# Kernel tuning notes

Hardware: AMD Instinct MI355X
Metric: run time of the kernel (lower is better)

Reference implementation:

```python
import jax, jax.numpy as jnp
import numpy as np

ANG = 5
WS = 8
HEADS = 2
REF = 2  # refPos = [2, 2]
NEG_SLOPE = 0.1
EPS = 1e-5


def _rel_pos_index(ws):
    coords = np.stack(np.meshgrid(np.arange(ws), np.arange(ws), indexing='ij'))  # [2,ws,ws]
    cf = coords.reshape(2, -1)
    rel = (cf[:, :, None] - cf[:, None, :]).transpose(1, 2, 0)  # [N,N,2]
    rel[..., 0] += ws - 1
    rel[..., 1] += ws - 1
    rel[..., 0] *= 2 * ws - 1
    return jnp.asarray(rel.sum(-1))  # [N,N] int

REL_IDX = _rel_pos_index(WS)


def _ln(x, g, b):
    m = jnp.mean(x, -1, keepdims=True)
    v = jnp.var(x, -1, keepdims=True)
    return (x - m) * jax.lax.rsqrt(v + EPS) * g + b


def setup_inputs():
    key = jax.random.key(0)
    ks = jax.random.split(key, 12)
    b, an2, c, h, w = 2, 25, 32, 96, 96
    C = 2 * c
    s = 0.02
    mlp_hidden = int(C * 4.0)
    inp = {}
    inp['global_fea'] = jax.random.normal(ks[0], (b, an2, c, h, w), jnp.float32)
    inp['centra_fea'] = jax.random.normal(ks[1], (b, c, h, w), jnp.float32)
    inp['disparity'] = jax.random.uniform(ks[2], (b, 1, h, w), jnp.float32)
    inp['qkv_w'] = jax.random.normal(ks[3], (3 * C, C), jnp.float32) * s
    inp['qkv_b'] = jnp.zeros((3 * C,), jnp.float32)
    inp['proj_w'] = jax.random.normal(ks[4], (C, C), jnp.float32) * s
    inp['proj_b'] = jnp.zeros((C,), jnp.float32)
    inp['rpb_table'] = jax.random.normal(ks[5], ((2 * WS - 1) ** 2, HEADS), jnp.float32) * s
    inp['ln1_g'] = jnp.ones((C,), jnp.float32)
    inp['ln1_b'] = jnp.zeros((C,), jnp.float32)
    inp['ln2_g'] = jnp.ones((C,), jnp.float32)
    inp['ln2_b'] = jnp.zeros((C,), jnp.float32)
    inp['fc1_w'] = jax.random.normal(ks[6], (mlp_hidden, C), jnp.float32) * s
    inp['fc1_b'] = jnp.zeros((mlp_hidden,), jnp.float32)
    inp['fc2_w'] = jax.random.normal(ks[7], (C, mlp_hidden), jnp.float32) * s
    inp['fc2_b'] = jnp.zeros((C,), jnp.float32)
    inp['conv_w'] = jax.random.normal(ks[8], (c, C), jnp.float32) * s  # 1x1 conv kernel squeezed
    inp['conv_b'] = jnp.zeros((c,), jnp.float32)
    return inp


def _warp(centra_fea, disparity):
    # back-projection: bilinear warp of the central (2,2) view to all ANG*ANG views
    b, c, h, w = centra_fea.shape
    d = disparity[:, 0]  # [b,h,w]
    ys, xs = jnp.meshgrid(jnp.arange(h, dtype=jnp.float32), jnp.arange(w, dtype=jnp.float32), indexing='ij')
    offs = jnp.asarray([[u - REF, v - REF] for u in range(ANG) for v in range(ANG)], jnp.float32)  # [an2,2]
    sy = ys[None, None] + d[:, None] * offs[None, :, 0, None, None]  # [b,an2,h,w]
    sx = xs[None, None] + d[:, None] * offs[None, :, 1, None, None]
    x0f = jnp.floor(sx)
    y0f = jnp.floor(sy)
    wx = sx - x0f
    wy = sy - y0f
    x0 = jnp.clip(x0f.astype(jnp.int32), 0, w - 1)
    x1 = jnp.clip(x0 + 1, 0, w - 1)
    y0 = jnp.clip(y0f.astype(jnp.int32), 0, h - 1)
    y1 = jnp.clip(y0 + 1, 0, h - 1)
    flat = centra_fea.reshape(b, c, h * w)
    an2 = ANG * ANG

    def gather(yi, xi):
        idx = (yi * w + xi).reshape(b, 1, -1)  # [b,1,an2*h*w]
        g = jnp.take_along_axis(flat, jnp.broadcast_to(idx, (b, c, an2 * h * w)), axis=2)
        return g.reshape(b, c, an2, h, w).transpose(0, 2, 1, 3, 4)  # [b,an2,c,h,w]

    wx_ = wx[:, :, None]
    wy_ = wy[:, :, None]
    return ((1 - wy_) * (1 - wx_) * gather(y0, x0) + (1 - wy_) * wx_ * gather(y0, x1)
            + wy_ * (1 - wx_) * gather(y1, x0) + wy_ * wx_ * gather(y1, x1))


def reference(global_fea, centra_fea, disparity, qkv_w, qkv_b, proj_w, proj_b, rpb_table,
              ln1_g, ln1_b, ln2_g, ln2_b, fc1_w, fc1_b, fc2_w, fc2_b, conv_w, conv_b):
    b, an2, c, h, w = global_fea.shape
    warped = _warp(centra_fea, disparity)
    x = jnp.concatenate([global_fea, warped], axis=2)  # [b,an2,2c,h,w]
    C = 2 * c
    B = b * an2
    # 'b an2 c h w -> (b an2) (h w) c'
    x = x.reshape(B, C, h, w).transpose(0, 2, 3, 1).reshape(B, h * w, C)
    # --- Swin transformer block (shift_size=0, iteration_idx=0) ---
    shortcut = x
    xn = _ln(x, ln1_g, ln1_b).reshape(B, h, w, C)
    nh, nw = h // WS, w // WS
    xw = xn.reshape(B, nh, WS, nw, WS, C).transpose(0, 1, 3, 2, 4, 5).reshape(B * nh * nw, WS * WS, C)
    nwins, N = xw.shape[0], WS * WS
    hd = C // HEADS
    qkv = (xw @ qkv_w.T + qkv_b).reshape(nwins, N, 3, HEADS, hd).transpose(2, 0, 3, 1, 4)
    q, k, v = qkv[0], qkv[1], qkv[2]  # [nwins, heads, N, hd]
    scale = hd ** -0.5
    attn = jnp.einsum('whnd,whmd->whnm', q * scale, k)
    bias = rpb_table[REL_IDX].transpose(2, 0, 1)  # [heads,N,N]
    attn = jax.nn.softmax(attn + bias[None], axis=-1)
    out = jnp.einsum('whnm,whmd->whnd', attn, v).transpose(0, 2, 1, 3).reshape(nwins, N, C)
    out = out @ proj_w.T + proj_b
    out = out.reshape(B, nh, nw, WS, WS, C).transpose(0, 1, 3, 2, 4, 5).reshape(B, h * w, C)
    x = shortcut + out
    xm = _ln(x, ln2_g, ln2_b)
    xm = jax.nn.gelu(xm @ fc1_w.T + fc1_b, approximate=False) @ fc2_w.T + fc2_b
    x = x + xm
    # '(b an2) (h w) c -> (b an2) c h w' then 1x1 conv fuse + LeakyReLU(0.1)
    x = x.reshape(B, h, w, C)
    y = jnp.einsum('bhwc,oc->bohw', x, conv_w) + conv_b[None, :, None, None]
    y = jnp.where(y >= 0, y, NEG_SLOPE * y)
    return y.reshape(b, an2, c, h, w)
```

## Files before the change

### kernel.cpp

```cpp
#include <hip/hip_runtime.h>
#include <hip/hip_bf16.h>
#include <math.h>

#define W_    96
#define HW_   9216
#define NWIN_ 144

typedef __attribute__((ext_vector_type(4))) float          f32x4;
typedef __attribute__((ext_vector_type(8))) __bf16         bf16x8;
typedef __attribute__((ext_vector_type(8))) unsigned short u16x8;

#define MFMA(a,b,c) __builtin_amdgcn_mfma_f32_16x16x32_bf16((a),(b),(c),0,0,0)

#define WOFF_QKV  0
#define WOFF_PROJ 12288
#define WOFF_FC1  16384
#define WOFF_FC2  32768
#define WOFF_CONV 49152
#define WTOT      51200
#define POFF_QKVB  0
#define POFF_PROJB 192
#define POFF_FC1B  256
#define POFF_FC2B  512
#define POFF_CONVB 576
#define POFF_RPB   608
#define POFF_LN1G  1058
#define POFF_LN1B  1122
#define POFF_LN2G  1186
#define POFF_LN2B  1250
#define PTOT       1314

template<typename T> __device__ __forceinline__ float ldv(const T* p, long i);
template<> __device__ __forceinline__ float ldv<float>(const float* p, long i){ return p[i]; }
template<> __device__ __forceinline__ float ldv<__hip_bfloat16>(const __hip_bfloat16* p, long i){ return __bfloat162float(p[i]); }

template<typename T> __device__ __forceinline__ void stv(T* p, long i, float v);
template<> __device__ __forceinline__ void stv<float>(float* p, long i, float v){ p[i] = v; }
template<> __device__ __forceinline__ void stv<__hip_bfloat16>(__hip_bfloat16* p, long i, float v){ p[i] = __float2bfloat16(v); }

__device__ __forceinline__ bf16x8 ldbf8(const __bf16* w){
    u16x8 u = *(const u16x8*)w;
    return __builtin_bit_cast(bf16x8, u);
}

__global__ void probe_kernel(const void* ln1g, int* flag){
    if (threadIdx.x == 0){
        unsigned u = *(const unsigned*)ln1g;
        *flag = (u == 0x3F803F80u) ? 1 : 0;
    }
}

template<typename T, int WANT>
__global__ __launch_bounds__(256) void convert_params(
    const int* __restrict__ flag,
    const T* qkvw, const T* qkvb, const T* projw, const T* projb, const T* rpb,
    const T* ln1g, const T* ln1b, const T* ln2g, const T* ln2b,
    const T* fc1w, const T* fc1b, const T* fc2w, const T* fc2b,
    const T* convw, const T* convb,
    __bf16* __restrict__ wbf, float* __restrict__ pf)
{
    if (*flag != WANT) return;
    int idx = blockIdx.x*256 + threadIdx.x;
    if (idx >= WTOT + PTOT) return;
    if      (idx < 12288) wbf[WOFF_QKV  + idx]          = (__bf16)ldv(qkvw, idx);
    else if (idx < 16384) wbf[WOFF_PROJ + (idx-12288)]  = (__bf16)ldv(projw, idx-12288);
    else if (idx < 32768) wbf[WOFF_FC1  + (idx-16384)]  = (__bf16)ldv(fc1w, idx-16384);
    else if (idx < 49152) wbf[WOFF_FC2  + (idx-32768)]  = (__bf16)ldv(fc2w, idx-32768);
    else if (idx < WTOT)  wbf[WOFF_CONV + (idx-49152)]  = (__bf16)ldv(convw, idx-49152);
    else {
        int p = idx - WTOT;
        if      (p < 192)  pf[POFF_QKVB  + p]        = ldv(qkvb, p);
        else if (p < 256)  pf[POFF_PROJB + (p-192)]  = ldv(projb, p-192);
        else if (p < 512)  pf[POFF_FC1B  + (p-256)]  = ldv(fc1b, p-256);
        else if (p < 576)  pf[POFF_FC2B  + (p-512)]  = ldv(fc2b, p-512);
        else if (p < 608)  pf[POFF_CONVB + (p-576)]  = ldv(convb, p-576);
        else if (p < 1058) pf[POFF_RPB   + (p-608)]  = ldv(rpb, p-608);
        else if (p < 1122) pf[POFF_LN1G  + (p-1058)] = ldv(ln1g, p-1058);
        else if (p < 1186) pf[POFF_LN1B  + (p-1122)] = ldv(ln1b, p-1122);
        else if (p < 1250) pf[POFF_LN2G  + (p-1186)] = ldv(ln2g, p-1186);
        else               pf[POFF_LN2B  + (p-1250)] = ldv(ln2b, p-1250);
    }
}

template<typename T, int WANT>
__global__ __launch_bounds__(256) void fused_kernel(
    const int* __restrict__ flag,
    const T* __restrict__ gf, const T* __restrict__ cf, const T* __restrict__ disp,
    const __bf16* __restrict__ wbf, const float* __restrict__ pf,
    T* __restrict__ out)
{
    if (*flag != WANT) return;
    __shared__ float  xs[64*65];
    __shared__ __bf16 arena[18432];

    const int tid  = threadIdx.x;
    const int lane = tid & 63, wid = tid >> 6;
    const int g = lane >> 4, cl = lane & 15;
    const int blk  = blockIdx.x;
    const int Bidx = blk / NWIN_;
    const int wrem = blk % NWIN_;
    const int wy = wrem / 12, wx = wrem % 12;
    const int b = Bidx / 25, a = Bidx % 25;
    const int hw00 = (wy*8)*W_ + wx*8;

    __bf16* qb  = arena;
    __bf16* kb  = arena + 4608;
    __bf16* vT  = arena + 9216;
    __bf16* xnr = arena + 13824;

    float* tile  = (float*)arena;
    float* tile2 = (float*)arena + 2112;
    int*   iy0 = (int*)((char*)arena + 16896);
    int*   iy1 = iy0 + 64;
    int*   ix0 = iy1 + 64;
    int*   ix1 = ix0 + 64;
    float* fys = (float*)(ix1 + 64);
    float* fxs = fys + 64;

    if (tid < 64){
        int ty = tid >> 3, tx = tid & 7;
        int y = wy*8 + ty, x = wx*8 + tx;
        int pix = y*W_ + x;
        float d  = ldv(disp, (long)b*HW_ + pix);
        float dy = (float)(a/5 - 2), dx = (float)(a%5 - 2);
        float sy = (float)y + d*dy, sx = (float)x + d*dx;
        float y0f = floorf(sy), x0f = floorf(sx);
        fys[tid] = sy - y0f; fxs[tid] = sx - x0f;
        int y0 = min(max((int)y0f,0), W_-1);
        int x0 = min(max((int)x0f,0), W_-1);
        iy0[tid]=y0; iy1[tid]=min(y0+1,W_-1);
        ix0[tid]=x0; ix1[tid]=min(x0+1,W_-1);
    }
    {
        int p = tid & 63;
        long pixoff = hw00 + (p>>3)*W_ + (p&7);
        for (int c = tid>>6; c < 32; c += 4)
            tile[c*66 + p] = ldv(gf, (((long)b*25 + a)*32 + c)*HW_ + pixoff);
    }
    __syncthreads();

    {
        int p = tid & 63;
        float fy = fys[p], fx = fxs[p];
        float w00=(1.f-fy)*(1.f-fx), w01=(1.f-fy)*fx, w10=fy*(1.f-fx), w11=fy*fx;
        long r0 = (long)iy0[p]*W_, r1 = (long)iy1[p]*W_;
        int xa = ix0[p], xb = ix1[p];
        for (int c = tid>>6; c < 32; c += 4){
            long cb = ((long)b*32 + c)*HW_;
            float v00 = ldv(cf, cb+r0+xa), v01 = ldv(cf, cb+r0+xb);
            float v10 = ldv(cf, cb+r1+xa), v11 = ldv(cf, cb+r1+xb);
            tile2[c*66 + p] = w00*v00 + w01*v01 + w10*v10 + w11*v11;
        }
    }
    __syncthreads();

    {
        const int t = tid>>2, quad = tid&3;
        float v[16]; float sum=0.f, sq=0.f;
        #pragma unroll
        for (int j=0;j<16;++j){
            int c = quad*16+j;
            float val = (c<32) ? tile[c*66 + t] : tile2[(c-32)*66 + t];
            v[j]=val; sum+=val; sq+=val*val;
        }
        sum += __shfl_xor(sum,1); sq += __shfl_xor(sq,1);
        sum += __shfl_xor(sum,2); sq += __shfl_xor(sq,2);
        float m  = sum*(1.f/64.f);
        float rs = rsqrtf(sq*(1.f/64.f) - m*m + 1e-5f);
        #pragma unroll
        for (int j=0;j<16;++j){
            int c = quad*16+j;
            xs[t*65 + c] = v[j];
            xnr[t*72 + c] = (__bf16)((v[j]-m)*rs*pf[POFF_LN1G+c] + pf[POFF_LN1B+c]);
        }
    }
    __syncthreads();

    {
        bf16x8 af[4][2];
        #pragma unroll
        for (int m=0;m<4;++m)
            #pragma unroll
            for (int ks=0;ks<2;++ks)
                af[m][ks] = *(const bf16x8*)(xnr + (16*m+cl)*72 + ks*32 + 8*g);
        f32x4 acc[3][4];
        #pragma unroll
        for (int nt=0;nt<3;++nt)
            #pragma unroll
            for (int m=0;m<4;++m) acc[nt][m] = (f32x4){0.f,0.f,0.f,0.f};
        const int f = wid*16 + cl;
        #pragma unroll
        for (int ks=0;ks<2;++ks)
            #pragma unroll
            for (int nt=0;nt<3;++nt){
                bf16x8 bw = ldbf8(wbf + WOFF_QKV + (long)(nt*64 + f)*64 + ks*32 + 8*g);
                #pragma unroll
                for (int m=0;m<4;++m) acc[nt][m] = MFMA(af[m][ks], bw, acc[nt][m]);
            }
        float bq = pf[POFF_QKVB + f], bk2 = pf[POFF_QKVB + 64 + f], bv2 = pf[POFF_QKVB + 128 + f];
        #pragma unroll
        for (int m=0;m<4;++m)
            #pragma unroll
            for (int r=0;r<4;++r){
                int t = 16*m + 4*g + r;
                qb[t*72 + f] = (__bf16)((acc[0][m][r] + bq)*0.1767766953f);
                kb[t*72 + f] = (__bf16)(acc[1][m][r] + bk2);
                vT[f*72 + t] = (__bf16)(acc[2][m][r] + bv2);
            }
    }
    __syncthreads();

    const int strip = wid*16;
    f32x4 sc[2][4];
    {
        bf16x8 aq0 = *(const bf16x8*)(qb + (strip+cl)*72 + 8*g);
        bf16x8 aq1 = *(const bf16x8*)(qb + (strip+cl)*72 + 32 + 8*g);
        #pragma unroll
        for (int h=0;h<2;++h)
            #pragma unroll
            for (int jt=0;jt<4;++jt){
                bf16x8 bk = *(const bf16x8*)(kb + (jt*16+cl)*72 + 32*h + 8*g);
                f32x4 z = {0.f,0.f,0.f,0.f};
                sc[h][jt] = MFMA(h?aq1:aq0, bk, z);
            }
    }
    __bf16* rpbs = xnr;
    for (int e=tid; e<450; e+=256) rpbs[e] = (__bf16)pf[POFF_RPB+e];
    __syncthreads();

    __bf16* pbuf = qb;
    __bf16* ob   = kb;
    #pragma unroll
    for (int h=0;h<2;++h){
        float inv[4];
        #pragma unroll
        for (int jt=0;jt<4;++jt)
            #pragma unroll
            for (int r=0;r<4;++r){
                int t = strip + 4*g + r, j = jt*16 + cl;
                int di = (t>>3)-(j>>3)+7, dj = (t&7)-(j&7)+7;
                sc[h][jt][r] += (float)rpbs[(di*15+dj)*2 + h];
            }
        #pragma unroll
        for (int r=0;r<4;++r){
            float m0 = fmaxf(fmaxf(sc[h][0][r],sc[h][1][r]),fmaxf(sc[h][2][r],sc[h][3][r]));
            m0 = fmaxf(m0,__shfl_xor(m0,1));
            m0 = fmaxf(m0,__shfl_xor(m0,2));
            m0 = fmaxf(m0,__shfl_xor(m0,4));
            m0 = fmaxf(m0,__shfl_xor(m0,8));
            float s=0.f;
            #pragma unroll
            for (int jt=0;jt<4;++jt){ float e=__expf(sc[h][jt][r]-m0); sc[h][jt][r]=e; s+=e; }
            s += __shfl_xor(s,1); s += __shfl_xor(s,2);
            s += __shfl_xor(s,4); s += __shfl_xor(s,8);
            inv[r] = 1.f/s;
        }
        #pragma unroll
        for (int jt=0;jt<4;++jt)
            #pragma unroll
            for (int r=0;r<4;++r)
                pbuf[(strip+4*g+r)*72 + jt*16+cl] = (__bf16)(sc[h][jt][r]*inv[r]);
        bf16x8 ap0 = *(const bf16x8*)(pbuf + (strip+cl)*72 + 8*g);
        bf16x8 ap1 = *(const bf16x8*)(pbuf + (strip+cl)*72 + 32 + 8*g);
        f32x4 ov[2];
        ov[0] = (f32x4){0.f,0.f,0.f,0.f};
        ov[1] = (f32x4){0.f,0.f,0.f,0.f};
        #pragma unroll
        for (int ks=0;ks<2;++ks)
            #pragma unroll
            for (int dt=0;dt<2;++dt){
                bf16x8 bv = *(const bf16x8*)(vT + (32*h + dt*16 + cl)*72 + ks*32 + 8*g);
                ov[dt] = MFMA(ks?ap1:ap0, bv, ov[dt]);
            }
        #pragma unroll
        for (int dt=0;dt<2;++dt)
            #pragma unroll
            for (int r=0;r<4;++r)
                ob[(strip+4*g+r)*72 + 32*h + dt*16 + cl] = (__bf16)(ov[dt][r]);
    }
    __syncthreads();

    {
        const int f = wid*16 + cl;
        f32x4 pacc[4];
        #pragma unroll
        for (int m=0;m<4;++m) pacc[m] = (f32x4){0.f,0.f,0.f,0.f};
        #pragma unroll
        for (int ks=0;ks<2;++ks){
            bf16x8 bw = ldbf8(wbf + WOFF_PROJ + (long)f*64 + ks*32 + 8*g);
            #pragma unroll
            for (int m=0;m<4;++m){
                bf16x8 ao = *(const bf16x8*)(ob + (16*m+cl)*72 + ks*32 + 8*g);
                pacc[m] = MFMA(ao, bw, pacc[m]);
            }
        }
        float pbias = pf[POFF_PROJB + f];
        #pragma unroll
        for (int m=0;m<4;++m)
            #pragma unroll
            for (int r=0;r<4;++r){
                int t = 16*m + 4*g + r;
                xs[t*65 + f] += pacc[m][r] + pbias;
            }
    }
    __syncthreads();

    __bf16* xn2 = vT;
    {
        const int t = tid>>2, quad = tid&3;
        float v[16]; float sum=0.f, sq=0.f;
        #pragma unroll
        for (int j=0;j<16;++j){
            float val = xs[t*65 + quad*16 + j];
            v[j]=val; sum+=val; sq+=val*val;
        }
        sum += __shfl_xor(sum,1); sq += __shfl_xor(sq,1);
        sum += __shfl_xor(sum,2); sq += __shfl_xor(sq,2);
        float m  = sum*(1.f/64.f);
        float rs = rsqrtf(sq*(1.f/64.f) - m*m + 1e-5f);
        #pragma unroll
        for (int j=0;j<16;++j){
            int c = quad*16+j;
            xn2[t*72 + c] = (__bf16)((v[j]-m)*rs*pf[POFF_LN2G+c] + pf[POFF_LN2B+c]);
        }
    }
    __syncthreads();

    __bf16* hb = arena;
    {
        bf16x8 af[4][2];
        #pragma unroll
        for (int m=0;m<4;++m)
            #pragma unroll
            for (int ks=0;ks<2;++ks)
                af[m][ks] = *(const bf16x8*)(xn2 + (16*m+cl)*72 + ks*32 + 8*g);
        const int f = wid*16 + cl;
        f32x4 acc2[4];
        #pragma unroll
        for (int m=0;m<4;++m) acc2[m] = (f32x4){0.f,0.f,0.f,0.f};
        #pragma unroll
        for (int half=0; half<2; ++half){
            f32x4 a1[2][4];
            #pragma unroll
            for (int nt=0;nt<2;++nt)
                #pragma unroll
                for (int m=0;m<4;++m) a1[nt][m] = (f32x4){0.f,0.f,0.f,0.f};
            #pragma unroll
            for (int ks=0;ks<2;++ks)
                #pragma unroll
                for (int nt=0;nt<2;++nt){
                    int hrow = half*128 + (2*wid+nt)*16 + cl;
                    bf16x8 bw = ldbf8(wbf + WOFF_FC1 + (long)hrow*64 + ks*32 + 8*g);
                    #pragma unroll
                    for (int m=0;m<4;++m) a1[nt][m] = MFMA(af[m][ks], bw, a1[nt][m]);
                }
            #pragma unroll
            for (int nt=0;nt<2;++nt){
                int hrow = half*128 + (2*wid+nt)*16 + cl;
                float hbias = pf[POFF_FC1B + hrow];
                #pragma unroll
                for (int m=0;m<4;++m)
                    #pragma unroll
                    for (int r=0;r<4;++r){
                        float vv = a1[nt][m][r] + hbias;
                        vv = 0.5f*vv*(1.f + erff(vv*0.70710678f));
                        hb[(16*m+4*g+r)*136 + (2*wid+nt)*16 + cl] = (__bf16)vv;
                    }
            }
            __syncthreads();
            #pragma unroll
            for (int ks=0;ks<4;++ks){
                bf16x8 bw = ldbf8(wbf + WOFF_FC2 + (long)f*256 + half*128 + ks*32 + 8*g);
                #pragma unroll
                for (int m=0;m<4;++m){
                    bf16x8 ah = *(const bf16x8*)(hb + (16*m+cl)*136 + ks*32 + 8*g);
                    acc2[m] = MFMA(ah, bw, acc2[m]);
                }
            }
            __syncthreads();
        }
        float b2 = pf[POFF_FC2B + f];
        #pragma unroll
        for (int m=0;m<4;++m)
            #pragma unroll
            for (int r=0;r<4;++r){
                int t = 16*m + 4*g + r;
                xs[t*65 + f] += acc2[m][r] + b2;
            }
    }
    __syncthreads();

    {
        const int nt = wid & 1, mh = wid >> 1;
        bf16x8 afr[2][2];
        #pragma unroll
        for (int mm=0;mm<2;++mm)
            #pragma unroll
            for (int ks=0;ks<2;++ks){
                int t = 16*(mh*2+mm) + cl;
                bf16x8 fr;
                #pragma unroll
                for (int i=0;i<8;++i) fr[i] = (__bf16)xs[t*65 + ks*32 + 8*g + i];
                afr[mm][ks] = fr;
            }
        f32x4 ca[2];
        ca[0] = (f32x4){0.f,0.f,0.f,0.f};
        ca[1] = (f32x4){0.f,0.f,0.f,0.f};
        #pragma unroll
        for (int ks=0;ks<2;++ks){
            bf16x8 bw = ldbf8(wbf + WOFF_CONV + (long)(nt*16+cl)*64 + ks*32 + 8*g);
            #pragma unroll
            for (int mm=0;mm<2;++mm) ca[mm] = MFMA(afr[mm][ks], bw, ca[mm]);
        }
        float cbias = pf[POFF_CONVB + nt*16 + cl];
        float* outs = (float*)arena;
        #pragma unroll
        for (int mm=0;mm<2;++mm)
            #pragma unroll
            for (int r=0;r<4;++r){
                int t = 16*(mh*2+mm) + 4*g + r;
                float vv = ca[mm][r] + cbias;
                vv = (vv >= 0.f) ? vv : 0.1f*vv;
                outs[(nt*16+cl)*68 + t] = vv;
            }
    }
    __syncthreads();

    {
        const int co = tid >> 3, seg = tid & 7;
        const float* outs = (const float*)arena;
        long obase = ((long)Bidx*32 + co)*HW_ + hw00 + (long)seg*W_;
        #pragma unroll
        for (int j=0;j<8;++j)
            stv(out, obase + j, outs[co*68 + seg*8 + j]);
    }
}

extern "C" void kernel_launch(void* const* d_in, const int* in_sizes, int n_in,
                              void* d_out, int out_size, void* d_ws, size_t ws_size,
                              hipStream_t stream)
{
    const void* gf    = d_in[0];
    const void* cf    = d_in[1];
    const void* disp  = d_in[2];
    const void* qkvw  = d_in[3];
    const void* qkvb  = d_in[4];
    const void* projw = d_in[5];
    const void* projb = d_in[6];
    const void* rpb   = d_in[7];
    const void* ln1g  = d_in[8];
    const void* ln1b  = d_in[9];
    const void* ln2g  = d_in[10];
    const void* ln2b  = d_in[11];
    const void* fc1w  = d_in[12];
    const void* fc1b  = d_in[13];
    const void* fc2w  = d_in[14];
    const void* fc2b  = d_in[15];
    const void* convw = d_in[16];
    const void* convb = d_in[17];

    int*    flag = (int*)d_ws;
    float*  pf   = (float*)((char*)d_ws + 512);
    __bf16* wbf  = (__bf16*)((char*)d_ws + 8192);

    probe_kernel<<<1, 64, 0, stream>>>(ln1g, flag);

    const int cgrid = (WTOT + PTOT + 255)/256;

    convert_params<float,0><<<cgrid,256,0,stream>>>(flag,
        (const float*)qkvw,(const float*)qkvb,(const float*)projw,(const float*)projb,
        (const float*)rpb,(const float*)ln1g,(const float*)ln1b,(const float*)ln2g,(const float*)ln2b,
        (const float*)fc1w,(const float*)fc1b,(const float*)fc2w,(const float*)fc2b,
        (const float*)convw,(const float*)convb, wbf, pf);
    fused_kernel<float,0><<<7200,256,0,stream>>>(flag,
        (const float*)gf,(const float*)cf,(const float*)disp, wbf, pf, (float*)d_out);

    using bf = __hip_bfloat16;
    convert_params<bf,1><<<cgrid,256,0,stream>>>(flag,
        (const bf*)qkvw,(const bf*)qkvb,(const bf*)projw,(const bf*)projb,
        (const bf*)rpb,(const bf*)ln1g,(const bf*)ln1b,(const bf*)ln2g,(const bf*)ln2b,
        (const bf*)fc1w,(const bf*)fc1b,(const bf*)fc2w,(const bf*)fc2b,
        (const bf*)convw,(const bf*)convb, wbf, pf);
    fused_kernel<bf,1><<<7200,256,0,stream>>>(flag,
        (const bf*)gf,(const bf*)cf,(const bf*)disp, wbf, pf, (bf*)d_out);
}
```

Baseline: 406.0 us.

## Merge dtype paths, shrink LDS with bf16 residual, precompute bias, fast GELU

Replaces the dual templated launches with one runtime-dtype kernel, which removes two of the four launches. The residual buffer is stored in bf16 instead of fp32 and the arena is shrunk to cut LDS use and raise occupancy. The relative-position bias is expanded to a dense table in the param kernel, erf-GELU is swapped for a polynomial approximation, block indices are swizzled for locality, and output stores are vectorized. The bf16 residual and the approximate GELU reduce numerical precision.

```diff
diff --git a/kernel.cpp b/kernel.cpp
--- a/kernel.cpp
+++ b/kernel.cpp
@@ -17,7 +17,9 @@
 #define WOFF_FC1  16384
 #define WOFF_FC2  32768
 #define WOFF_CONV 49152
+#define WOFF_BIAS 51200
 #define WTOT      51200
+#define BIAS_N    8192
 #define POFF_QKVB  0
 #define POFF_PROJB 192
 #define POFF_FC1B  256
@@ -30,17 +32,21 @@
 #define POFF_LN2B  1250
 #define PTOT       1314
 
-template<typename T> __device__ __forceinline__ float ldv(const T* p, long i);
-template<> __device__ __forceinline__ float ldv<float>(const float* p, long i){ return p[i]; }
-template<> __device__ __forceinline__ float ldv<__hip_bfloat16>(const __hip_bfloat16* p, long i){ return __bfloat162float(p[i]); }
-
-template<typename T> __device__ __forceinline__ void stv(T* p, long i, float v);
-template<> __device__ __forceinline__ void stv<float>(float* p, long i, float v){ p[i] = v; }
-template<> __device__ __forceinline__ void stv<__hip_bfloat16>(__hip_bfloat16* p, long i, float v){ p[i] = __float2bfloat16(v); }
-
+__device__ __forceinline__ float ldin(const void* p, long i, int isbf){
+    return isbf ? __bfloat162float(((const __hip_bfloat16*)p)[i]) : ((const float*)p)[i];
+}
 __device__ __forceinline__ bf16x8 ldbf8(const __bf16* w){
     u16x8 u = *(const u16x8*)w;
     return __builtin_bit_cast(bf16x8, u);
+}
+
+__device__ __forceinline__ float gelu_f(float v){
+    float u = fabsf(v) * 0.70710678f;
+    float t = __builtin_amdgcn_rcpf(1.f + 0.47047f*u);
+    float p = t*(0.3480242f + t*(-0.0958798f + t*0.7478556f));
+    float er = 1.f - p*__expf(-u*u);
+    er = copysignf(er, v);
+    return 0.5f*v*(1.f + er);
 }
 
 __global__ void probe_kernel(const void* ln1g, int* flag){
@@ -50,78 +56,55 @@
     }
 }
 
-template<typename T, int WANT>
 __global__ __launch_bounds__(256) void convert_params(
     const int* __restrict__ flag,
-    const T* qkvw, const T* qkvb, const T* projw, const T* projb, const T* rpb,
-    const T* ln1g, const T* ln1b, const T* ln2g, const T* ln2b,
-    const T* fc1w, const T* fc1b, const T* fc2w, const T* fc2b,
-    const T* convw, const T* convb,
+    const void* qkvw, const void* qkvb, const void* projw, const void* projb, const void* rpb,
+    const void* ln1g, const void* ln1b, const void* ln2g, const void* ln2b,
+    const void* fc1w, const void* fc1b, const void* fc2w, const void* fc2b,
+    const void* convw, const void* convb,
     __bf16* __restrict__ wbf, float* __restrict__ pf)
 {
-    if (*flag != WANT) return;
+    const int isbf = *flag;
     int idx = blockIdx.x*256 + threadIdx.x;
-    if (idx >= WTOT + PTOT) return;
-    if      (idx < 12288) wbf[WOFF_QKV  + idx]          = (__bf16)ldv(qkvw, idx);
-    else if (idx < 16384) wbf[WOFF_PROJ + (idx-12288)]  = (__bf16)ldv(projw, idx-12288);
-    else if (idx < 32768) wbf[WOFF_FC1  + (idx-16384)]  = (__bf16)ldv(fc1w, idx-16384);
-    else if (idx < 49152) wbf[WOFF_FC2  + (idx-32768)]  = (__bf16)ldv(fc2w, idx-32768);
-    else if (idx < WTOT)  wbf[WOFF_CONV + (idx-49152)]  = (__bf16)ldv(convw, idx-49152);
-    else {
+    if (idx >= WTOT + PTOT + BIAS_N) return;
+    if (idx < WTOT){
+        if      (idx < 12288) wbf[WOFF_QKV  + idx]          = (__bf16)ldin(qkvw, idx, isbf);
+        else if (idx < 16384) wbf[WOFF_PROJ + (idx-12288)]  = (__bf16)ldin(projw, idx-12288, isbf);
+        else if (idx < 32768) wbf[WOFF_FC1  + (idx-16384)]  = (__bf16)ldin(fc1w, idx-16384, isbf);
+        else if (idx < 49152) wbf[WOFF_FC2  + (idx-32768)]  = (__bf16)ldin(fc2w, idx-32768, isbf);
+        else                  wbf[WOFF_CONV + (idx-49152)]  = (__bf16)ldin(convw, idx-49152, isbf);
+    } else if (idx < WTOT + PTOT){
         int p = idx - WTOT;
-        if      (p < 192)  pf[POFF_QKVB  + p]        = ldv(qkvb, p);
-        else if (p < 256)  pf[POFF_PROJB + (p-192)]  = ldv(projb, p-192);
-        else if (p < 512)  pf[POFF_FC1B  + (p-256)]  = ldv(fc1b, p-256);
-        else if (p < 576)  pf[POFF_FC2B  + (p-512)]  = ldv(fc2b, p-512);
-        else if (p < 608)  pf[POFF_CONVB + (p-576)]  = ldv(convb, p-576);
-        else if (p < 1058) pf[POFF_RPB   + (p-608)]  = ldv(rpb, p-608);
-        else if (p < 1122) pf[POFF_LN1G  + (p-1058)] = ldv(ln1g, p-1058);
-        else if (p < 1186) pf[POFF_LN1B  + (p-1122)] = ldv(ln1b, p-1122);
-        else if (p < 1250) pf[POFF_LN2G  + (p-1186)] = ldv(ln2g, p-1186);
-        else               pf[POFF_LN2B  + (p-1250)] = ldv(ln2b, p-1250);
-    }
-}
-
-template<typename T, int WANT>
-__global__ __launch_bounds__(256) void fused_kernel(
-    const int* __restrict__ flag,
-    const T* __restrict__ gf, const T* __restrict__ cf, const T* __restrict__ disp,
-    const __bf16* __restrict__ wbf, const float* __restrict__ pf,
-    T* __restrict__ out)
+        if      (p < 192)  pf[POFF_QKVB  + p]        = ldin(qkvb, p, isbf);
+        else if (p < 256)  pf[POFF_PROJB + (p-192)]  = ldin(projb, p-192, isbf);
+        else if (p < 512)  pf[POFF_FC1B  + (p-256)]  = ldin(fc1b, p-256, isbf);
+        else if (p < 576)  pf[POFF_FC2B  + (p-512)]  = ldin(fc2b, p-512, isbf);
+        else if (p < 608)  pf[POFF_CONVB + (p-576)]  = ldin(convb, p-576, isbf);
+        else if (p < 1058) pf[POFF_RPB   + (p-608)]  = ldin(rpb, p-608, isbf);
+        else if (p < 1122) pf[POFF_LN1G  + (p-1058)] = ldin(ln1g, p-1058, isbf);
+        else if (p < 1186) pf[POFF_LN1B  + (p-1122)] = ldin(ln1b, p-1122, isbf);
+        else if (p < 1250) pf[POFF_LN2G  + (p-1186)] = ldin(ln2g, p-1186, isbf);
+        else               pf[POFF_LN2B  + (p-1250)] = ldin(ln2b, p-1250, isbf);
+    } else {
+        int eb = idx - (WTOT + PTOT);
+        int h = eb >> 12, rem = eb & 4095;
+        int i = rem >> 6, j = rem & 63;
+        int di = (i>>3)-(j>>3)+7, dj = (i&7)-(j&7)+7;
+        wbf[WOFF_BIAS + eb] = (__bf16)ldin(rpb, (di*15+dj)*2 + h, isbf);
+    }
+}
+
+template<typename T>
+__device__ __forceinline__ void phaseA0(
+    const T* gf, const T* disp,
+    float* tile, int* iy0,int* iy1,int* ix0,int* ix1,float* fys,float* fxs,
+    int tid,int b,int a,int wy,int wx,int hw00)
 {
-    if (*flag != WANT) return;
-    __shared__ float  xs[64*65];
-    __shared__ __bf16 arena[18432];
-
-    const int tid  = threadIdx.x;
-    const int lane = tid & 63, wid = tid >> 6;
-    const int g = lane >> 4, cl = lane & 15;
-    const int blk  = blockIdx.x;
-    const int Bidx = blk / NWIN_;
-    const int wrem = blk % NWIN_;
-    const int wy = wrem / 12, wx = wrem % 12;
-    const int b = Bidx / 25, a = Bidx % 25;
-    const int hw00 = (wy*8)*W_ + wx*8;
-
-    __bf16* qb  = arena;
-    __bf16* kb  = arena + 4608;
-    __bf16* vT  = arena + 9216;
-    __bf16* xnr = arena + 13824;
-
-    float* tile  = (float*)arena;
-    float* tile2 = (float*)arena + 2112;
-    int*   iy0 = (int*)((char*)arena + 16896);
-    int*   iy1 = iy0 + 64;
-    int*   ix0 = iy1 + 64;
-    int*   ix1 = ix0 + 64;
-    float* fys = (float*)(ix1 + 64);
-    float* fxs = fys + 64;
-
     if (tid < 64){
         int ty = tid >> 3, tx = tid & 7;
         int y = wy*8 + ty, x = wx*8 + tx;
         int pix = y*W_ + x;
-        float d  = ldv(disp, (long)b*HW_ + pix);
+        float d = (float)disp[(long)b*HW_ + pix];
         float dy = (float)(a/5 - 2), dx = (float)(a%5 - 2);
         float sy = (float)y + d*dy, sx = (float)x + d*dx;
         float y0f = floorf(sy), x0f = floorf(sx);
@@ -131,27 +114,73 @@
         iy0[tid]=y0; iy1[tid]=min(y0+1,W_-1);
         ix0[tid]=x0; ix1[tid]=min(x0+1,W_-1);
     }
-    {
-        int p = tid & 63;
-        long pixoff = hw00 + (p>>3)*W_ + (p&7);
-        for (int c = tid>>6; c < 32; c += 4)
-            tile[c*66 + p] = ldv(gf, (((long)b*25 + a)*32 + c)*HW_ + pixoff);
-    }
-    __syncthreads();
-
-    {
-        int p = tid & 63;
-        float fy = fys[p], fx = fxs[p];
-        float w00=(1.f-fy)*(1.f-fx), w01=(1.f-fy)*fx, w10=fy*(1.f-fx), w11=fy*fx;
-        long r0 = (long)iy0[p]*W_, r1 = (long)iy1[p]*W_;
-        int xa = ix0[p], xb = ix1[p];
-        for (int c = tid>>6; c < 32; c += 4){
-            long cb = ((long)b*32 + c)*HW_;
-            float v00 = ldv(cf, cb+r0+xa), v01 = ldv(cf, cb+r0+xb);
-            float v10 = ldv(cf, cb+r1+xa), v11 = ldv(cf, cb+r1+xb);
-            tile2[c*66 + p] = w00*v00 + w01*v01 + w10*v10 + w11*v11;
-        }
-    }
+    int p = tid & 63;
+    long pixoff = hw00 + (p>>3)*W_ + (p&7);
+    for (int c = tid>>6; c < 32; c += 4)
+        tile[c*67 + p] = (float)gf[(((long)b*25 + a)*32 + c)*HW_ + pixoff];
+}
+
+template<typename T>
+__device__ __forceinline__ void phaseA1(
+    const T* cf, float* tile2,
+    const int* iy0,const int* iy1,const int* ix0,const int* ix1,const float* fys,const float* fxs,
+    int tid,int b)
+{
+    int p = tid & 63;
+    float fy = fys[p], fx = fxs[p];
+    float w00=(1.f-fy)*(1.f-fx), w01=(1.f-fy)*fx, w10=fy*(1.f-fx), w11=fy*fx;
+    long r0 = (long)iy0[p]*W_, r1 = (long)iy1[p]*W_;
+    int xa = ix0[p], xb = ix1[p];
+    for (int c = tid>>6; c < 32; c += 4){
+        long cb = ((long)b*32 + c)*HW_;
+        float v00 = (float)cf[cb+r0+xa], v01 = (float)cf[cb+r0+xb];
+        float v10 = (float)cf[cb+r1+xa], v11 = (float)cf[cb+r1+xb];
+        tile2[c*67 + p] = w00*v00 + w01*v01 + w10*v10 + w11*v11;
+    }
+}
+
+__global__ __launch_bounds__(256) void fused_kernel(
+    const int* __restrict__ flag,
+    const void* __restrict__ gf, const void* __restrict__ cf, const void* __restrict__ disp,
+    const __bf16* __restrict__ wbf, const float* __restrict__ pf,
+    void* __restrict__ out)
+{
+    __shared__ __bf16 xs[64*72];
+    __shared__ __bf16 arena[14336];
+
+    const int isbf = *flag;
+    const int tid  = threadIdx.x;
+    const int lane = tid & 63, wid = tid >> 6;
+    const int g = lane >> 4, cl = lane & 15;
+    const int bid  = blockIdx.x;
+    const int blk  = (bid & 7)*900 + (bid >> 3);
+    const int Bidx = blk / NWIN_;
+    const int wrem = blk % NWIN_;
+    const int wy = wrem / 12, wx = wrem % 12;
+    const int b = Bidx / 25, a = Bidx % 25;
+    const int hw00 = (wy*8)*W_ + wx*8;
+
+    __bf16* qb  = arena;
+    __bf16* kb  = arena + 4608;
+    __bf16* vT  = arena + 9216;
+    __bf16* xn  = arena + 9728;
+
+    float* tile  = (float*)arena;
+    float* tile2 = tile + 2144;
+    int*   iy0 = (int*)((char*)arena + 17408);
+    int*   iy1 = iy0 + 64;
+    int*   ix0 = iy1 + 64;
+    int*   ix1 = ix0 + 64;
+    float* fys = (float*)(ix1 + 64);
+    float* fxs = fys + 64;
+
+    if (isbf) phaseA0((const __hip_bfloat16*)gf, (const __hip_bfloat16*)disp,
+                      tile, iy0,iy1,ix0,ix1,fys,fxs, tid,b,a,wy,wx,hw00);
+    else      phaseA0((const float*)gf, (const float*)disp,
+                      tile, iy0,iy1,ix0,ix1,fys,fxs, tid,b,a,wy,wx,hw00);
+    __syncthreads();
+    if (isbf) phaseA1((const __hip_bfloat16*)cf, tile2, iy0,iy1,ix0,ix1,fys,fxs, tid,b);
+    else      phaseA1((const float*)cf, tile2, iy0,iy1,ix0,ix1,fys,fxs, tid,b);
     __syncthreads();
 
     {
@@ -160,19 +189,26 @@
         #pragma unroll
         for (int j=0;j<16;++j){
             int c = quad*16+j;
-            float val = (c<32) ? tile[c*66 + t] : tile2[(c-32)*66 + t];
+            float val = (c<32) ? tile[c*67 + t] : tile2[(c-32)*67 + t];
             v[j]=val; sum+=val; sq+=val*val;
         }
         sum += __shfl_xor(sum,1); sq += __shfl_xor(sq,1);
         sum += __shfl_xor(sum,2); sq += __shfl_xor(sq,2);
         float m  = sum*(1.f/64.f);
         float rs = rsqrtf(sq*(1.f/64.f) - m*m + 1e-5f);
-        #pragma unroll
-        for (int j=0;j<16;++j){
-            int c = quad*16+j;
-            xs[t*65 + c] = v[j];
-            xnr[t*72 + c] = (__bf16)((v[j]-m)*rs*pf[POFF_LN1G+c] + pf[POFF_LN1B+c]);
-        }
+        bf16x8 s0,s1,n0,n1;
+        #pragma unroll
+        for (int j=0;j<8;++j){
+            int c0 = quad*16+j, c1 = quad*16+8+j;
+            s0[j] = (__bf16)v[j];
+            s1[j] = (__bf16)v[8+j];
+            n0[j] = (__bf16)((v[j]  -m)*rs*pf[POFF_LN1G+c0] + pf[POFF_LN1B+c0]);
+            n1[j] = (__bf16)((v[8+j]-m)*rs*pf[POFF_LN1G+c1] + pf[POFF_LN1B+c1]);
+        }
+        *(bf16x8*)(xs + t*72 + quad*16)     = s0;
+        *(bf16x8*)(xs + t*72 + quad*16 + 8) = s1;
+        *(bf16x8*)(xn + t*72 + quad*16)     = n0;
+        *(bf16x8*)(xn + t*72 + quad*16 + 8) = n1;
     }
     __syncthreads();
 
@@ -182,7 +218,8 @@
         for (int m=0;m<4;++m)
             #pragma unroll
             for (int ks=0;ks<2;++ks)
-                af[m][ks] = *(const bf16x8*)(xnr + (16*m+cl)*72 + ks*32 + 8*g);
+                af[m][ks] = *(const bf16x8*)(xn + (16*m+cl)*72 + ks*32 + 8*g);
+        __syncthreads();
         f32x4 acc[3][4];
         #pragma unroll
         for (int nt=0;nt<3;++nt)
@@ -223,9 +260,15 @@
                 f32x4 z = {0.f,0.f,0.f,0.f};
                 sc[h][jt] = MFMA(h?aq1:aq0, bk, z);
             }
-    }
-    __bf16* rpbs = xnr;
-    for (int e=tid; e<450; e+=256) rpbs[e] = (__bf16)pf[POFF_RPB+e];
+        const __bf16* bptr = wbf + WOFF_BIAS + (strip + 4*g)*64 + cl;
+        #pragma unroll
+        for (int h=0;h<2;++h)
+            #pragma unroll
+            for (int jt=0;jt<4;++jt)
+                #pragma unroll
+                for (int r=0;r<4;++r)
+                    sc[h][jt][r] += (float)bptr[h*4096 + r*64 + jt*16];
+    }
     __syncthreads();
 
     __bf16* pbuf = qb;
@@ -233,14 +276,6 @@
     #pragma unroll
     for (int h=0;h<2;++h){
         float inv[4];
-        #pragma unroll
-        for (int jt=0;jt<4;++jt)
-            #pragma unroll
-            for (int r=0;r<4;++r){
-                int t = strip + 4*g + r, j = jt*16 + cl;
-                int di = (t>>3)-(j>>3)+7, dj = (t&7)-(j&7)+7;
-                sc[h][jt][r] += (float)rpbs[(di*15+dj)*2 + h];
-            }
         #pragma unroll
         for (int r=0;r<4;++r){
             float m0 = fmaxf(fmaxf(sc[h][0][r],sc[h][1][r]),fmaxf(sc[h][2][r],sc[h][3][r]));
@@ -300,29 +335,35 @@
             #pragma unroll
             for (int r=0;r<4;++r){
                 int t = 16*m + 4*g + r;
-                xs[t*65 + f] += pacc[m][r] + pbias;
-            }
-    }
-    __syncthreads();
-
-    __bf16* xn2 = vT;
+                float y = (float)xs[t*72 + f] + pacc[m][r] + pbias;
+                xs[t*72 + f] = (__bf16)y;
+            }
+    }
+    __syncthreads();
+
+    __bf16* xn2 = arena + 9728;
     {
         const int t = tid>>2, quad = tid&3;
+        bf16x8 r0 = *(const bf16x8*)(xs + t*72 + quad*16);
+        bf16x8 r1 = *(const bf16x8*)(xs + t*72 + quad*16 + 8);
         float v[16]; float sum=0.f, sq=0.f;
         #pragma unroll
-        for (int j=0;j<16;++j){
-            float val = xs[t*65 + quad*16 + j];
-            v[j]=val; sum+=val; sq+=val*val;
-        }
+        for (int j=0;j<8;++j){ v[j] = (float)r0[j]; v[8+j] = (float)r1[j]; }
+        #pragma unroll
+        for (int j=0;j<16;++j){ sum += v[j]; sq += v[j]*v[j]; }
         sum += __shfl_xor(sum,1); sq += __shfl_xor(sq,1);
         sum += __shfl_xor(sum,2); sq += __shfl_xor(sq,2);
         float m  = sum*(1.f/64.f);
         float rs = rsqrtf(sq*(1.f/64.f) - m*m + 1e-5f);
-        #pragma unroll
-        for (int j=0;j<16;++j){
-            int c = quad*16+j;
-            xn2[t*72 + c] = (__bf16)((v[j]-m)*rs*pf[POFF_LN2G+c] + pf[POFF_LN2B+c]);
-        }
+        bf16x8 n0,n1;
+        #pragma unroll
+        for (int j=0;j<8;++j){
+            int c0 = quad*16+j, c1 = quad*16+8+j;
+            n0[j] = (__bf16)((v[j]  -m)*rs*pf[POFF_LN2G+c0] + pf[POFF_LN2B+c0]);
+            n1[j] = (__bf16)((v[8+j]-m)*rs*pf[POFF_LN2G+c1] + pf[POFF_LN2B+c1]);
+        }
+        *(bf16x8*)(xn2 + t*72 + quad*16)     = n0;
+        *(bf16x8*)(xn2 + t*72 + quad*16 + 8) = n1;
     }
     __syncthreads();
 
@@ -362,8 +403,7 @@
                 for (int m=0;m<4;++m)
                     #pragma unroll
                     for (int r=0;r<4;++r){
-                        float vv = a1[nt][m][r] + hbias;
-                        vv = 0.5f*vv*(1.f + erff(vv*0.70710678f));
+                        float vv = gelu_f(a1[nt][m][r] + hbias);
                         hb[(16*m+4*g+r)*136 + (2*wid+nt)*16 + cl] = (__bf16)vv;
                     }
             }
@@ -385,24 +425,14 @@
             #pragma unroll
             for (int r=0;r<4;++r){
                 int t = 16*m + 4*g + r;
-                xs[t*65 + f] += acc2[m][r] + b2;
+                float y = (float)xs[t*72 + f] + acc2[m][r] + b2;
+                xs[t*72 + f] = (__bf16)y;
             }
     }
     __syncthreads();
 
     {
         const int nt = wid & 1, mh = wid >> 1;
-        bf16x8 afr[2][2];
-        #pragma unroll
-        for (int mm=0;mm<2;++mm)
-            #pragma unroll
-            for (int ks=0;ks<2;++ks){
-                int t = 16*(mh*2+mm) + cl;
-                bf16x8 fr;
-                #pragma unroll
-                for (int i=0;i<8;++i) fr[i] = (__bf16)xs[t*65 + ks*32 + 8*g + i];
-                afr[mm][ks] = fr;
-            }
         f32x4 ca[2];
         ca[0] = (f32x4){0.f,0.f,0.f,0.f};
         ca[1] = (f32x4){0.f,0.f,0.f,0.f};
@@ -410,7 +440,10 @@
         for (int ks=0;ks<2;++ks){
             bf16x8 bw = ldbf8(wbf + WOFF_CONV + (long)(nt*16+cl)*64 + ks*32 + 8*g);
             #pragma unroll
-            for (int mm=0;mm<2;++mm) ca[mm] = MFMA(afr[mm][ks], bw, ca[mm]);
+            for (int mm=0;mm<2;++mm){
+                bf16x8 afr = *(const bf16x8*)(xs + (16*(mh*2+mm)+cl)*72 + ks*32 + 8*g);
+                ca[mm] = MFMA(afr, bw, ca[mm]);
+            }
         }
         float cbias = pf[POFF_CONVB + nt*16 + cl];
         float* outs = (float*)arena;
@@ -430,9 +463,18 @@
         const int co = tid >> 3, seg = tid & 7;
         const float* outs = (const float*)arena;
         long obase = ((long)Bidx*32 + co)*HW_ + hw00 + (long)seg*W_;
-        #pragma unroll
-        for (int j=0;j<8;++j)
-            stv(out, obase + j, outs[co*68 + seg*8 + j]);
+        if (isbf){
+            bf16x8 vb;
+            #pragma unroll
+            for (int j=0;j<8;++j) vb[j] = (__bf16)outs[co*68 + seg*8 + j];
+            *(bf16x8*)((__hip_bfloat16*)out + obase) = vb;
+        } else {
+            f32x4 va, vb2;
+            #pragma unroll
+            for (int j=0;j<4;++j){ va[j] = outs[co*68 + seg*8 + j]; vb2[j] = outs[co*68 + seg*8 + 4 + j]; }
+            *(f32x4*)((float*)out + obase)     = va;
+            *(f32x4*)((float*)out + obase + 4) = vb2;
+        }
     }
 }
 
@@ -465,22 +507,10 @@
 
     probe_kernel<<<1, 64, 0, stream>>>(ln1g, flag);
 
-    const int cgrid = (WTOT + PTOT + 255)/256;
-
-    convert_params<float,0><<<cgrid,256,0,stream>>>(flag,
-        (const float*)qkvw,(const float*)qkvb,(const float*)projw,(const float*)projb,
-        (const float*)rpb,(const float*)ln1g,(const float*)ln1b,(const float*)ln2g,(const float*)ln2b,
-        (const float*)fc1w,(const float*)fc1b,(const float*)fc2w,(const float*)fc2b,
-        (const float*)convw,(const float*)convb, wbf, pf);
-    fused_kernel<float,0><<<7200,256,0,stream>>>(flag,
-        (const float*)gf,(const float*)cf,(const float*)disp, wbf, pf, (float*)d_out);
-
-    using bf = __hip_bfloat16;
-    convert_params<bf,1><<<cgrid,256,0,stream>>>(flag,
-        (const bf*)qkvw,(const bf*)qkvb,(const bf*)projw,(const bf*)projb,
-        (const bf*)rpb,(const bf*)ln1g,(const bf*)ln1b,(const bf*)ln2g,(const bf*)ln2b,
-        (const bf*)fc1w,(const bf*)fc1b,(const bf*)fc2w,(const bf*)fc2b,
-        (const bf*)convw,(const bf*)convb, wbf, pf);
-    fused_kernel<bf,1><<<7200,256,0,stream>>>(flag,
-        (const bf*)gf,(const bf*)cf,(const bf*)disp, wbf, pf, (bf*)d_out);
-}
+    const int cgrid = (WTOT + PTOT + BIAS_N + 255)/256;
+    convert_params<<<cgrid,256,0,stream>>>(flag,
+        qkvw,qkvb,projw,projb,rpb,ln1g,ln1b,ln2g,ln2b,
+        fc1w,fc1b,fc2w,fc2b,convw,convb, wbf, pf);
+
+    fused_kernel<<<7200,256,0,stream>>>(flag, gf, cf, disp, wbf, pf, d_out);
+}
```

After: 390.8 us. 3.8% less time.
